# Performance work log

Hardware: AMD Instinct MI355X
Metric: run time of the kernel (lower is better)

Reference implementation:

```python
import jax, jax.numpy as jnp
import numpy as np

H = 64  # hidden size


def _gru_cell(x, h, Wih, Whh, bih, bhh):
    """PyTorch-convention GRU cell. x:[B,in], h:[B,H]. Gate order: r, z, n."""
    gi = x @ Wih.T + bih              # [B, 3H]
    gh = h @ Whh.T + bhh              # [B, 3H]
    ir, iz, in_ = jnp.split(gi, 3, axis=-1)
    hr, hz, hn = jnp.split(gh, 3, axis=-1)
    r = jax.nn.sigmoid(ir + hr)
    z = jax.nn.sigmoid(iz + hz)
    n = jnp.tanh(in_ + r * hn)
    return (1.0 - z) * n + z * h


def setup_inputs() -> dict:
    key = jax.random.key(0)
    B, T, NIN = 4096, 256, 6
    ks = jax.random.split(key, 24)

    def w(k, shape, fan):
        return (jax.random.normal(k, shape, jnp.float32) / np.sqrt(fan).astype(np.float32))

    inp = {"x": jax.random.normal(ks[0], (B, T, NIN), jnp.float32)}
    # encoder layer 0 (input 6) and layer 1 (input 64)
    inp["enc_Wih0"] = w(ks[1], (3 * H, NIN), H)
    inp["enc_Whh0"] = w(ks[2], (3 * H, H), H)
    inp["enc_bih0"] = w(ks[3], (3 * H,), H)
    inp["enc_bhh0"] = w(ks[4], (3 * H,), H)
    inp["enc_Wih1"] = w(ks[5], (3 * H, H), H)
    inp["enc_Whh1"] = w(ks[6], (3 * H, H), H)
    inp["enc_bih1"] = w(ks[7], (3 * H,), H)
    inp["enc_bhh1"] = w(ks[8], (3 * H,), H)
    # decoder layer 0 (input 1) and layer 1 (input 64)
    inp["dec_Wih0"] = w(ks[9], (3 * H, 1), H)
    inp["dec_Whh0"] = w(ks[10], (3 * H, H), H)
    inp["dec_bih0"] = w(ks[11], (3 * H,), H)
    inp["dec_bhh0"] = w(ks[12], (3 * H,), H)
    inp["dec_Wih1"] = w(ks[13], (3 * H, H), H)
    inp["dec_Whh1"] = w(ks[14], (3 * H, H), H)
    inp["dec_bih1"] = w(ks[15], (3 * H,), H)
    inp["dec_bhh1"] = w(ks[16], (3 * H,), H)
    # output head
    inp["out_W"] = w(ks[17], (1, H), H)
    inp["out_b"] = w(ks[18], (1,), H)
    inp["target_len"] = 180
    return inp


def reference(x, enc_Wih0, enc_Whh0, enc_bih0, enc_bhh0,
              enc_Wih1, enc_Whh1, enc_bih1, enc_bhh1,
              dec_Wih0, dec_Whh0, dec_bih0, dec_bhh0,
              dec_Wih1, dec_Whh1, dec_bih1, dec_bhh1,
              out_W, out_b, target_len):
    B = x.shape[0]
    dtype = x.dtype

    # ---- encoder: 2-layer GRU over x, return final hidden per layer ----
    seq = jnp.swapaxes(x, 0, 1)  # [T, B, 6] time-major
    enc_layers = [(enc_Wih0, enc_Whh0, enc_bih0, enc_bhh0),
                  (enc_Wih1, enc_Whh1, enc_bih1, enc_bhh1)]
    h_finals = []
    for (Wih, Whh, bih, bhh) in enc_layers:
        def step(h, xt, Wih=Wih, Whh=Whh, bih=bih, bhh=bhh):
            hn = _gru_cell(xt, h, Wih, Whh, bih, bhh)
            return hn, hn
        h_last, seq = jax.lax.scan(step, jnp.zeros((B, H), dtype), seq)
        h_finals.append(h_last)

    def dec_step(carry, _):
        h0, h1, prev = carry
        h0 = _gru_cell(prev, h0, dec_Wih0, dec_Whh0, dec_bih0, dec_bhh0)
        h1 = _gru_cell(h0, h1, dec_Wih1, dec_Whh1, dec_bih1, dec_bhh1)
        cv = h1 @ out_W.T + out_b  # [B, 1]
        return (h0, h1, cv), cv

    prev0 = jnp.zeros((B, 1), dtype)
    _, outs = jax.lax.scan(dec_step, (h_finals[0], h_finals[1], prev0),
                           None, length=target_len)
    return jnp.swapaxes(outs, 0, 1)  # [B, target_len, 1]
```

## Files before the change

### kernel.cpp

```cpp
#include <hip/hip_runtime.h>
#include <cstdint>

typedef _Float16 half8 __attribute__((ext_vector_type(8)));
typedef _Float16 half4v __attribute__((ext_vector_type(4)));
typedef __attribute__((ext_vector_type(4))) float floatx4;
typedef __attribute__((ext_vector_type(2))) float float2v;

#define TSEQ 256
#define TDEC 180
#define NIN  6
#define GROWS 16
#define NBLK (4096 / GROWS)
#define NSL 4
#define RS0 104
#define RS1 72
#define L2E 1.4426950408889634f

__device__ __forceinline__ floatx4 mfma16(half8 a, half8 b, floatx4 c) {
  return __builtin_amdgcn_mfma_f32_16x16x32_f16(a, b, c, 0, 0, 0);
}

__device__ __forceinline__ half8 ldh8(const _Float16* p) { return *(const half8*)p; }

#define PASS2_I3(F0, F1, r, z, g, W, QR, QZ, QG) do {                   \
  r = mfma16(W[0][0], F0, QR); z = mfma16(W[1][0], F0, QZ); g = mfma16(W[2][0], F0, QG); \
  r = mfma16(W[0][1], F1, r);  z = mfma16(W[1][1], F1, z);  g = mfma16(W[2][1], F1, g);  \
} while (0)

#define PASS2_A2I1(F0, F1, r, z, g, W, QG) do {                         \
  r = mfma16(W[0][0], F0, r); z = mfma16(W[1][0], F0, z); g = mfma16(W[2][0], F0, QG); \
  r = mfma16(W[0][1], F1, r); z = mfma16(W[1][1], F1, z); g = mfma16(W[2][1], F1, g);  \
} while (0)

#define PASS1_I1(F0, r, z, g, W3, QG) do {                              \
  r = mfma16(W3[0], F0, r); z = mfma16(W3[1], F0, z); g = mfma16(W3[2], F0, QG); \
} while (0)

#define SYNC() do {                                         \
  asm volatile("s_waitcnt lgkmcnt(0)" ::: "memory");        \
  __builtin_amdgcn_s_barrier();                             \
  asm volatile("" ::: "memory");                            \
} while (0)

__global__ void __launch_bounds__(512, 2)
gru_persist(const float* __restrict__ x,
            const float* __restrict__ eWih0, const float* __restrict__ eWhh0,
            const float* __restrict__ ebih0, const float* __restrict__ ebhh0,
            const float* __restrict__ eWih1, const float* __restrict__ eWhh1,
            const float* __restrict__ ebih1, const float* __restrict__ ebhh1,
            const float* __restrict__ dWih0, const float* __restrict__ dWhh0,
            const float* __restrict__ dbih0, const float* __restrict__ dbhh0,
            const float* __restrict__ dWih1, const float* __restrict__ dWhh1,
            const float* __restrict__ dbih1, const float* __restrict__ dbhh1,
            const float* __restrict__ outW, const float* __restrict__ outB,
            float* __restrict__ out)
{
  __shared__ __align__(16) _Float16 s0[NSL][16][RS0];
  __shared__ __align__(16) _Float16 s1[NSL][16][RS1];

  const int tid  = threadIdx.x;
  const bool isA = tid < 256;
  const int wvL  = (tid >> 6) & 3;
  const int lane = tid & 63;
  const int c    = lane & 15;
  const int q    = lane >> 4;
  const int u    = wvL * 16 + c;
  const int ub   = wvL * 16 + q * 4;
  const long base = (long)blockIdx.x * GROWS;

  for (int i = tid; i < NSL * 16 * RS0; i += 512) ((uint16_t*)s0)[i] = 0;
  for (int i = tid; i < NSL * 16 * RS1; i += 512) ((uint16_t*)s1)[i] = 0;
  if (tid < GROWS * NIN) {
    int m = tid / 6, i2 = tid - m * 6;
    s0[0][m][64 + i2] = (_Float16)x[(base + m) * (TSEQ * NIN) + i2];
  }

  half8 W1[3][2], W2[3][2];
  half8 W2e[3];
  half8 W1d[3][2], W2d[3][2];
  float hr[4] = {0, 0, 0, 0};
  const float SC[3] = {L2E, L2E, 2.0f * L2E};

  auto loadW64 = [&](const float* W, half8 (&D)[3][2]) {
    #pragma unroll
    for (int s = 0; s < 3; s++) {
      const int n = (s * 4 + wvL) * 16 + c;
      #pragma unroll
      for (int kt = 0; kt < 2; kt++) {
        const int k0 = kt * 32 + q * 8;
        #pragma unroll
        for (int j = 0; j < 8; j++) D[s][kt][j] = (_Float16)(SC[s] * W[n * 64 + k0 + j]);
      }
    }
  };

  auto NLIN = [&](const floatx4 R, const floatx4 Z, const floatx4 GIN, const floatx4 GHN,
                  _Float16* dst) {
    half4v hv;
    #pragma unroll
    for (int pr = 0; pr < 2; pr++) {
      const int e = pr * 2;
      float2v er, ez;
      er.x = __builtin_amdgcn_exp2f(-R[e]);   er.y = __builtin_amdgcn_exp2f(-R[e + 1]);
      ez.x = __builtin_amdgcn_exp2f(-Z[e]);   ez.y = __builtin_amdgcn_exp2f(-Z[e + 1]);
      const float2v Dr = 1.0f + er, Dz = 1.0f + ez;
      const float2v P  = Dr * Dz;
      float2v rp;
      rp.x = __builtin_amdgcn_rcpf(P.x);      rp.y = __builtin_amdgcn_rcpf(P.y);
      const float2v gr = rp * Dz, gz = rp * Dr;
      const float2v gin = {GIN[e], GIN[e + 1]}, ghn = {GHN[e], GHN[e + 1]};
      const float2v vn = gin + gr * ghn;
      float2v en;
      en.x = __builtin_amdgcn_exp2f(-vn.x);   en.y = __builtin_amdgcn_exp2f(-vn.y);
      const float2v Dn = 1.0f + en;
      const float rpn = __builtin_amdgcn_rcpf(Dn.x * Dn.y);
      const float2v dsw = {Dn.y, Dn.x};
      const float2v nn = (2.0f * rpn) * dsw - 1.0f;
      const float2v hold = {hr[e], hr[e + 1]};
      const float2v hn = nn + gz * (hold - nn);
      hr[e] = hn.x; hr[e + 1] = hn.y;
      hv[e] = (_Float16)hn.x; hv[e + 1] = (_Float16)hn.y;
    }
    *(half4v*)dst = hv;
  };

  const float ob = outB[0];
  floatx4 QR, QZ, Q3, Q4;
  floatx4 DRv, DZv, D3v, D4v;
  floatx4 TRv, TZv, T3v, T4v;
  float wk[2][8];
  if (isA) {
    loadW64(eWhh0, W1);
    #pragma unroll
    for (int s = 0; s < 3; s++) {
      const int n = (s * 4 + wvL) * 16 + c;
      #pragma unroll
      for (int j = 0; j < 8; j++) {
        float v = (q == 0 && j < NIN) ? SC[s] * eWih0[n * NIN + j] : 0.0f;
        W2e[s][j] = (_Float16)v;
      }
    }
    loadW64(dWhh0, W1d);
    #pragma unroll
    for (int s = 0; s < 3; s++) {
      const int n = (s * 4 + wvL) * 16 + c;
      const float wd = SC[s] * dWih0[n];
      #pragma unroll
      for (int kt = 0; kt < 2; kt++) {
        const int k0 = kt * 32 + q * 8;
        #pragma unroll
        for (int j = 0; j < 8; j++) W2d[s][kt][j] = (_Float16)(wd * outW[k0 + j]);
      }
    }
    #pragma unroll
    for (int r = 0; r < 4; r++) {
      const int g = ub + r;
      QR[r] = L2E * (ebih0[g] + ebhh0[g]);
      QZ[r] = L2E * (ebih0[64 + g] + ebhh0[64 + g]);
      Q3[r] = 2.0f * L2E * ebhh0[128 + g];
      Q4[r] = 2.0f * L2E * ebih0[128 + g];
      TRv[r] = L2E * (dbih0[g] + dbhh0[g]);
      TZv[r] = L2E * (dbih0[64 + g] + dbhh0[64 + g]);
      T3v[r] = 2.0f * L2E * dbhh0[128 + g];
      T4v[r] = 2.0f * L2E * dbih0[128 + g];
      DRv[r] = TRv[r] + L2E * (dWih0[g] * ob);
      DZv[r] = TZv[r] + L2E * (dWih0[64 + g] * ob);
      D3v[r] = T3v[r];
      D4v[r] = T4v[r] + 2.0f * L2E * (dWih0[128 + g] * ob);
    }
  } else {
    loadW64(eWih1, W1); loadW64(eWhh1, W2);
    loadW64(dWih1, W1d); loadW64(dWhh1, W2d);
    #pragma unroll
    for (int r = 0; r < 4; r++) {
      const int g = ub + r;
      QR[r] = L2E * (ebih1[g] + ebhh1[g]);
      QZ[r] = L2E * (ebih1[64 + g] + ebhh1[64 + g]);
      Q3[r] = 2.0f * L2E * ebih1[128 + g];
      Q4[r] = 2.0f * L2E * ebhh1[128 + g];
      DRv[r] = L2E * (dbih1[g] + dbhh1[g]);
      DZv[r] = L2E * (dbih1[64 + g] + dbhh1[64 + g]);
      D3v[r] = 2.0f * L2E * dbih1[128 + g];
      D4v[r] = 2.0f * L2E * dbhh1[128 + g];
    }
    #pragma unroll
    for (int kt = 0; kt < 2; kt++)
      #pragma unroll
      for (int j = 0; j < 8; j++) wk[kt][j] = outW[kt * 32 + q * 8 + j];
  }
  __syncthreads();

  if (isA) {
    const bool doX = (lane < 24);
    const float *px0 = nullptr;
    int xo0 = 0;
    float xa0 = 0.f, xb0 = 0.f;
    if (doX) {
      int s_ = wvL * 24 + lane;
      int m0 = s_ / 6, i0 = s_ - m0 * 6;
      px0 = x + (base + m0) * (TSEQ * NIN) + i0;
      xo0 = m0 * RS0 + 64 + i0;
      xa0 = px0[NIN];
      xb0 = px0[2 * NIN];
    }
    for (int k = 0; k < TSEQ; k += 4) {
      #pragma unroll
      for (int h4 = 0; h4 < 4; h4++) {
        const int i_ = k + h4, p = h4, pn = (h4 + 1) & 3;
        const half8 a0 = ldh8(&s0[p][c][q * 8]);
        const half8 a1 = ldh8(&s0[p][c][32 + q * 8]);
        const half8 xf = ldh8(&s0[p][c][64 + q * 8]);
        floatx4 aR = QR, aZ = QZ, a3 = Q3, a4 = Q4;
        {
          floatx4 tR, tZ, tG;
          PASS2_I3(a0, a1, tR, tZ, tG, W1, aR, aZ, a3);
          aR = tR; aZ = tZ; a3 = tG;
        }
        PASS1_I1(xf, aR, aZ, a4, W2e, a4);
        if (doX && i_ + 1 < TSEQ) {
          ((_Float16*)s0[pn])[xo0] = (_Float16)xa0;
          xa0 = xb0;
          if (i_ + 3 < TSEQ) xb0 = px0[(i_ + 3) * NIN];
        }
        NLIN(aR, aZ, a4, a3, &s0[pn][c][ub]);
        SYNC();
      }
    }
    {
      const half8 a0 = ldh8(&s0[0][c][q * 8]);
      const half8 a1 = ldh8(&s0[0][c][32 + q * 8]);
      floatx4 aR, aZ, a3;
      PASS2_I3(a0, a1, aR, aZ, a3, W1d, TRv, TZv, T3v);
      NLIN(aR, aZ, T4v, a3, &s0[1][c][ub]);
      SYNC();
    }
    for (int i_ = TSEQ + 1; i_ < TSEQ + TDEC; i_++) {
      const int p = i_ & 3, pn = (i_ + 1) & 3;
      const half8 a0 = ldh8(&s0[p][c][q * 8]);
      const half8 a1 = ldh8(&s0[p][c][32 + q * 8]);
      floatx4 aR, aZ, a3, a4;
      PASS2_I3(a0, a1, aR, aZ, a3, W1d, DRv, DZv, D3v);
      SYNC();
      const half8 b0 = ldh8(&s1[p][c][q * 8]);
      const half8 b1 = ldh8(&s1[p][c][32 + q * 8]);
      PASS2_A2I1(b0, b1, aR, aZ, a4, W2d, D4v);
      NLIN(aR, aZ, a4, a3, &s0[pn][c][ub]);
      SYNC();
    }
    SYNC();
  } else {
    for (int k = 0; k < TSEQ; k += 4) {
      #pragma unroll
      for (int h4 = 0; h4 < 4; h4++) {
        const int kk = k + h4;
        if (kk > 0) {
          const int p = (h4 + 3) & 3, pn = h4;
          const half8 f0 = ldh8(&s1[p][c][q * 8]);
          const half8 f1 = ldh8(&s1[p][c][32 + q * 8]);
          floatx4 aR, aZ, a3, a4;
          PASS2_I3(f0, f1, aR, aZ, a4, W2, QR, QZ, Q4);
          const half8 g0 = ldh8(&s0[pn][c][q * 8]);
          const half8 g1 = ldh8(&s0[pn][c][32 + q * 8]);
          PASS2_A2I1(g0, g1, aR, aZ, a3, W1, Q3);
          NLIN(aR, aZ, a3, a4, &s1[pn][c][ub]);
        }
        SYNC();
      }
    }
    {
      const half8 f0 = ldh8(&s1[3][c][q * 8]);
      const half8 f1 = ldh8(&s1[3][c][32 + q * 8]);
      floatx4 aR, aZ, a3, a4;
      PASS2_I3(f0, f1, aR, aZ, a4, W2, QR, QZ, Q4);
      const half8 g0 = ldh8(&s0[0][c][q * 8]);
      const half8 g1 = ldh8(&s0[0][c][32 + q * 8]);
      PASS2_A2I1(g0, g1, aR, aZ, a3, W1, Q3);
      NLIN(aR, aZ, a3, a4, &s1[0][c][ub]);
      SYNC();
    }
    {
      const half8 f0 = ldh8(&s1[0][c][q * 8]);
      const half8 f1 = ldh8(&s1[0][c][32 + q * 8]);
      floatx4 aR, aZ, a3, a4;
      PASS2_I3(f0, f1, aR, aZ, a4, W2d, DRv, DZv, D4v);
      const half8 g0 = ldh8(&s0[1][c][q * 8]);
      const half8 g1 = ldh8(&s0[1][c][32 + q * 8]);
      PASS2_A2I1(g0, g1, aR, aZ, a3, W1d, D3v);
      NLIN(aR, aZ, a3, a4, &s1[1][c][ub]);
      SYNC();
    }
    for (int i_ = TSEQ + 1; i_ < TSEQ + TDEC; i_++) {
      const int p = i_ & 3, pn = (i_ + 1) & 3;
      const half8 f0 = ldh8(&s1[p][c][q * 8]);
      const half8 f1 = ldh8(&s1[p][c][32 + q * 8]);
      floatx4 aR, aZ, a3, a4;
      PASS2_I3(f0, f1, aR, aZ, a4, W2d, DRv, DZv, D4v);
      if (wvL == 0) {
        float cv = 0.0f;
        #pragma unroll
        for (int j = 0; j < 8; j++) {
          cv = fmaf((float)f0[j], wk[0][j], cv);
          cv = fmaf((float)f1[j], wk[1][j], cv);
        }
        cv += __shfl_xor(cv, 16);
        cv += __shfl_xor(cv, 32);
        if (lane < 16) out[(base + lane) * TDEC + (i_ - TSEQ - 1)] = cv + ob;
      }
      SYNC();
      const half8 g0 = ldh8(&s0[pn][c][q * 8]);
      const half8 g1 = ldh8(&s0[pn][c][32 + q * 8]);
      PASS2_A2I1(g0, g1, aR, aZ, a3, W1d, D3v);
      NLIN(aR, aZ, a3, a4, &s1[pn][c][ub]);
      SYNC();
    }
    if (wvL == 0) {
      const half8 f0 = ldh8(&s1[0][c][q * 8]);
      const half8 f1 = ldh8(&s1[0][c][32 + q * 8]);
      float cv = 0.0f;
      #pragma unroll
      for (int j = 0; j < 8; j++) {
        cv = fmaf((float)f0[j], wk[0][j], cv);
        cv = fmaf((float)f1[j], wk[1][j], cv);
      }
      cv += __shfl_xor(cv, 16);
      cv += __shfl_xor(cv, 32);
      if (lane < 16) out[(base + lane) * TDEC + (TDEC - 1)] = cv + ob;
    }
  }
}

extern "C" void kernel_launch(void* const* d_in, const int* in_sizes, int n_in,
                              void* d_out, int out_size, void* d_ws, size_t ws_size,
                              hipStream_t stream) {
  (void)in_sizes; (void)n_in; (void)d_ws; (void)ws_size; (void)out_size;
  const float* x     = (const float*)d_in[0];
  const float* eWih0 = (const float*)d_in[1];
  const float* eWhh0 = (const float*)d_in[2];
  const float* ebih0 = (const float*)d_in[3];
  const float* ebhh0 = (const float*)d_in[4];
  const float* eWih1 = (const float*)d_in[5];
  const float* eWhh1 = (const float*)d_in[6];
  const float* ebih1 = (const float*)d_in[7];
  const float* ebhh1 = (const float*)d_in[8];
  const float* dWih0 = (const float*)d_in[9];
  const float* dWhh0 = (const float*)d_in[10];
  const float* dbih0 = (const float*)d_in[11];
  const float* dbhh0 = (const float*)d_in[12];
  const float* dWih1 = (const float*)d_in[13];
  const float* dWhh1 = (const float*)d_in[14];
  const float* dbih1 = (const float*)d_in[15];
  const float* dbhh1 = (const float*)d_in[16];
  const float* outW  = (const float*)d_in[17];
  const float* outB  = (const float*)d_in[18];
  hipLaunchKernelGGL(gru_persist, dim3(NBLK), dim3(512), 0, stream,
                     x, eWih0, eWhh0, ebih0, ebhh0, eWih1, eWhh1, ebih1, ebhh1,
                     dWih0, dWhh0, dbih0, dbhh0, dWih1, dWhh1, dbih1, dbhh1,
                     outW, outB, (float*)d_out);
}
```

Before: 346.8 us.

## Replace encoder block barriers with LDS progress-counter flags between producer/consumer waves

In the encoder phase, the per-step workgroup barriers between the layer-0 waves and the layer-1 waves are replaced by shared-memory progress counters. Each wave increments its group's counter after writing its hidden state, and consumers spin on the counters until the required step is published. The 4-slot ring buffer lets layer 0 run up to three steps ahead of layer 1, decoupling the two layers' pipelines. This risks memory-ordering issues with plain LDS stores versus the atomic, plus spin-wait overhead that competes for issue slots.

New measurement: 352.9 us. Within noise of the previous version (+1.7%).

```diff
diff --git a/kernel.cpp b/kernel.cpp
--- a/kernel.cpp
+++ b/kernel.cpp
@@ -5,6 +5,7 @@
 typedef _Float16 half4v __attribute__((ext_vector_type(4)));
 typedef __attribute__((ext_vector_type(4))) float floatx4;
 typedef __attribute__((ext_vector_type(2))) float float2v;
+typedef unsigned int uint;
 
 #define TSEQ 256
 #define TDEC 180
@@ -41,6 +42,12 @@
   __builtin_amdgcn_s_barrier();                             \
   asm volatile("" ::: "memory");                            \
 } while (0)
+
+__device__ __forceinline__ void pollge(const volatile uint* p, uint need) {
+  while (*p < need) { }
+  asm volatile("" ::: "memory");
+}
+#define PUBLISH() do { asm volatile("" ::: "memory"); if (lane == 0) atomicAdd(myctr, 1u); } while (0)
 
 __global__ void __launch_bounds__(512, 2)
 gru_persist(const float* __restrict__ x,
@@ -57,6 +64,7 @@
 {
   __shared__ __align__(16) _Float16 s0[NSL][16][RS0];
   __shared__ __align__(16) _Float16 s1[NSL][16][RS1];
+  __shared__ __align__(16) uint prog[16];
 
   const int tid  = threadIdx.x;
   const bool isA = tid < 256;
@@ -64,12 +72,16 @@
   const int lane = tid & 63;
   const int c    = lane & 15;
   const int q    = lane >> 4;
-  const int u    = wvL * 16 + c;
   const int ub   = wvL * 16 + q * 4;
   const long base = (long)blockIdx.x * GROWS;
 
+  const volatile uint* vA = (const volatile uint*)&prog[0];
+  const volatile uint* vB = (const volatile uint*)&prog[8];
+  uint* myctr = (uint*)&prog[isA ? 0 : 8];
+
   for (int i = tid; i < NSL * 16 * RS0; i += 512) ((uint16_t*)s0)[i] = 0;
   for (int i = tid; i < NSL * 16 * RS1; i += 512) ((uint16_t*)s1)[i] = 0;
+  if (tid < 16) prog[tid] = 0;
   if (tid < GROWS * NIN) {
     int m = tid / 6, i2 = tid - m * 6;
     s0[0][m][64 + i2] = (_Float16)x[(base + m) * (TSEQ * NIN) + i2];
@@ -207,6 +219,7 @@
       #pragma unroll
       for (int h4 = 0; h4 < 4; h4++) {
         const int i_ = k + h4, p = h4, pn = (h4 + 1) & 3;
+        pollge(vA, 4u * (uint)i_);
         const half8 a0 = ldh8(&s0[p][c][q * 8]);
         const half8 a1 = ldh8(&s0[p][c][32 + q * 8]);
         const half8 xf = ldh8(&s0[p][c][64 + q * 8]);
@@ -217,15 +230,18 @@
           aR = tR; aZ = tZ; a3 = tG;
         }
         PASS1_I1(xf, aR, aZ, a4, W2e, a4);
+        pollge(vB, i_ > 3 ? 4u * (uint)(i_ - 3) : 0u);
         if (doX && i_ + 1 < TSEQ) {
           ((_Float16*)s0[pn])[xo0] = (_Float16)xa0;
           xa0 = xb0;
           if (i_ + 3 < TSEQ) xb0 = px0[(i_ + 3) * NIN];
         }
         NLIN(aR, aZ, a4, a3, &s0[pn][c][ub]);
-        SYNC();
-      }
-    }
+        PUBLISH();
+      }
+    }
+    pollge(vA, 4u * (uint)TSEQ);
+    pollge(vB, 4u * (uint)(TSEQ - 3));
     {
       const half8 a0 = ldh8(&s0[0][c][q * 8]);
       const half8 a1 = ldh8(&s0[0][c][32 + q * 8]);
@@ -252,32 +268,21 @@
     for (int k = 0; k < TSEQ; k += 4) {
       #pragma unroll
       for (int h4 = 0; h4 < 4; h4++) {
-        const int kk = k + h4;
-        if (kk > 0) {
-          const int p = (h4 + 3) & 3, pn = h4;
-          const half8 f0 = ldh8(&s1[p][c][q * 8]);
-          const half8 f1 = ldh8(&s1[p][c][32 + q * 8]);
-          floatx4 aR, aZ, a3, a4;
-          PASS2_I3(f0, f1, aR, aZ, a4, W2, QR, QZ, Q4);
-          const half8 g0 = ldh8(&s0[pn][c][q * 8]);
-          const half8 g1 = ldh8(&s0[pn][c][32 + q * 8]);
-          PASS2_A2I1(g0, g1, aR, aZ, a3, W1, Q3);
-          NLIN(aR, aZ, a3, a4, &s1[pn][c][ub]);
-        }
-        SYNC();
-      }
-    }
-    {
-      const half8 f0 = ldh8(&s1[3][c][q * 8]);
-      const half8 f1 = ldh8(&s1[3][c][32 + q * 8]);
-      floatx4 aR, aZ, a3, a4;
-      PASS2_I3(f0, f1, aR, aZ, a4, W2, QR, QZ, Q4);
-      const half8 g0 = ldh8(&s0[0][c][q * 8]);
-      const half8 g1 = ldh8(&s0[0][c][32 + q * 8]);
-      PASS2_A2I1(g0, g1, aR, aZ, a3, W1, Q3);
-      NLIN(aR, aZ, a3, a4, &s1[0][c][ub]);
-      SYNC();
-    }
+        const int j_ = k + h4, p = h4, pn = (h4 + 1) & 3;
+        pollge(vB, 4u * (uint)j_);
+        const half8 f0 = ldh8(&s1[p][c][q * 8]);
+        const half8 f1 = ldh8(&s1[p][c][32 + q * 8]);
+        floatx4 aR, aZ, a3, a4;
+        PASS2_I3(f0, f1, aR, aZ, a4, W2, QR, QZ, Q4);
+        pollge(vA, 4u * (uint)(j_ + 1));
+        const half8 g0 = ldh8(&s0[pn][c][q * 8]);
+        const half8 g1 = ldh8(&s0[pn][c][32 + q * 8]);
+        PASS2_A2I1(g0, g1, aR, aZ, a3, W1, Q3);
+        NLIN(aR, aZ, a3, a4, &s1[pn][c][ub]);
+        PUBLISH();
+      }
+    }
+    SYNC();
     {
       const half8 f0 = ldh8(&s1[0][c][q * 8]);
       const half8 f1 = ldh8(&s1[0][c][32 + q * 8]);
```
